# Optimization experiments

Hardware: AMD Instinct MI355X
Metric: run time of the kernel (lower is better)

## Reference

```python
import jax, jax.numpy as jnp
import numpy as np

N_HEAD = 12
N_EMBD = 768


def setup_inputs() -> dict:
    key = jax.random.key(0)
    k1, k2, k3, k4, k5 = jax.random.split(key, 5)
    B, T, C = 4, 2048, N_EMBD
    s = 0.02
    x = jax.random.normal(k1, (B, T, C), dtype=jnp.float32)
    w_attn = jax.random.normal(k2, (C, 3 * C), dtype=jnp.float32) * s
    b_attn = jnp.zeros((3 * C,), dtype=jnp.float32)
    w_proj = jax.random.normal(k3, (C, C), dtype=jnp.float32) * s
    b_proj = jnp.zeros((C,), dtype=jnp.float32)
    return {"x": x, "w_attn": w_attn, "b_attn": b_attn, "w_proj": w_proj, "b_proj": b_proj}


def reference(x, w_attn, b_attn, w_proj, b_proj):
    # dropout omitted (eval mode / dropout=0.0)
    B, T, C = x.shape
    H = N_HEAD
    D = C // H  # head dim
    qkv = x @ w_attn + b_attn                      # [B,T,3C]
    q, k, v = jnp.split(qkv, 3, axis=-1)
    q = q.reshape(B, T, H, D).transpose(0, 2, 1, 3)  # [B,H,T,D]
    k = k.reshape(B, T, H, D).transpose(0, 2, 1, 3)
    v = v.reshape(B, T, H, D).transpose(0, 2, 1, 3)
    att = jnp.einsum('bhqd,bhkd->bhqk', q, k) * (1.0 / np.sqrt(D))  # [B,H,T,T]
    causal = jnp.tril(jnp.ones((T, T), dtype=bool))
    att = jnp.where(causal[None, None], att, -jnp.inf)
    att = jax.nn.softmax(att, axis=-1)
    y = jnp.einsum('bhqk,bhkd->bhqd', att, v)      # [B,H,T,D]
    y = y.transpose(0, 2, 1, 3).reshape(B, T, C)
    return y @ w_proj + b_proj
```

## Files before the change

kernel.cpp:

```cpp
#include <hip/hip_runtime.h>
#include <stdint.h>

typedef unsigned short ushort_t;

#define T_SEQ 2048
#define BATCH 4
#define NHEAD 12
#define CEMB 768
#define HDIM 64
#define C3 2304

__device__ __forceinline__ ushort_t f2b_hw(float f) {
  union { __bf16 h; ushort_t u; } p;
  p.h = (__bf16)f;
  return p.u;
}
__device__ __forceinline__ uint32_t pkbf16(float lo, float hi) {
  union { __bf16 h[2]; uint32_t u; } p;
  p.h[0] = (__bf16)lo; p.h[1] = (__bf16)hi;
  return p.u;
}

typedef __attribute__((address_space(3))) unsigned int lds_u32_t;
typedef const __attribute__((address_space(1))) unsigned int glb_u32_t;
__device__ __forceinline__ void async_cp16(const void* g, void* l) {
  __builtin_amdgcn_global_load_lds((glb_u32_t*)g, (lds_u32_t*)l, 16, 0, 0);
}

__global__ __launch_bounds__(256) void prep_k(const float* __restrict__ x, ushort_t* __restrict__ xb,
                                              const float* __restrict__ wa, ushort_t* __restrict__ wT,
                                              const float* __restrict__ wp, ushort_t* __restrict__ wpT) {
  const int blk = blockIdx.x;
  const int tid = threadIdx.x;
  if (blk < 3072) {
    const int i = blk * 256 + tid;
    float4 a = ((const float4*)x)[2 * i];
    float4 b = ((const float4*)x)[2 * i + 1];
    uint4 v;
    v.x = pkbf16(a.x, a.y); v.y = pkbf16(a.z, a.w);
    v.z = pkbf16(b.x, b.y); v.w = pkbf16(b.z, b.w);
    ((uint4*)xb)[i] = v;
    return;
  }
  __shared__ ushort_t tile[32][33];
  const float* in; ushort_t* out; int R, C, bx, by;
  if (blk < 4800) {
    const int t = blk - 3072;
    in = wa; out = wT; R = CEMB; C = C3;
    bx = t % 72; by = t / 72;
  } else {
    const int t = blk - 4800;
    in = wp; out = wpT; R = CEMB; C = CEMB;
    bx = t % 24; by = t / 24;
  }
  const int tx = tid & 31, ty = tid >> 5;
  const int c0 = bx * 32, r0 = by * 32;
  for (int i = ty; i < 32; i += 8)
    tile[i][tx] = f2b_hw(in[(size_t)(r0 + i) * C + c0 + tx]);
  __syncthreads();
  for (int i = ty; i < 32; i += 8)
    out[(size_t)(c0 + i) * R + r0 + tx] = tile[tx][i];
}

typedef __bf16 bf16x8 __attribute__((ext_vector_type(8)));
typedef float f32x4 __attribute__((ext_vector_type(4)));

template <bool OUTF, int BM>
__global__ __launch_bounds__(256) void gemm_bt(const ushort_t* __restrict__ A,
                                               const ushort_t* __restrict__ Bt,
                                               const float* __restrict__ bias,
                                               void* __restrict__ Cv,
                                               int M, int N, int K) {
  constexpr int TM = BM / 32;
  __shared__ ushort_t As[2][BM * 32];
  __shared__ ushort_t Bs[2][128 * 32];
  const int tid = threadIdx.x;
  const int m0 = blockIdx.y * BM, n0 = blockIdx.x * 128;
  const int wid = tid >> 6, lane = tid & 63;
  const int quad = lane >> 4, l15 = lane & 15;
  const int wm = (wid >> 1) * (BM / 2), wn = (wid & 1) * 64;
  f32x4 acc[TM][4] = {};

  const int e0 = tid * 8;
  const int r0s = e0 >> 5, c0s = e0 & 31;
  const int e1 = e0 + 2048;
  const int r1s = e1 >> 5, c1s = e1 & 31;

  const int KS = K >> 5;

#define GSTAGE(ks, bf)                                                              \
  {                                                                                 \
    const int kc = (ks) << 5;                                                       \
    async_cp16(&A[(size_t)(m0 + r0s) * K + kc + c0s], &As[bf][e0]);                 \
    if constexpr (BM == 128)                                                        \
      async_cp16(&A[(size_t)(m0 + r1s) * K + kc + c1s], &As[bf][e1]);               \
    async_cp16(&Bt[(size_t)(n0 + r0s) * K + kc + c0s], &Bs[bf][e0]);                \
    async_cp16(&Bt[(size_t)(n0 + r1s) * K + kc + c1s], &Bs[bf][e1]);                \
  }

  GSTAGE(0, 0);
  for (int ks = 0; ks < KS; ks++) {
    const int pb = ks & 1;
    __syncthreads();
    if (ks + 1 < KS) GSTAGE(ks + 1, pb ^ 1);
    bf16x8 af[TM], bfr[4];
#pragma unroll
    for (int t = 0; t < TM; t++)
      af[t] = *(const bf16x8*)&As[pb][(wm + t * 16 + l15) * 32 + quad * 8];
#pragma unroll
    for (int t = 0; t < 4; t++)
      bfr[t] = *(const bf16x8*)&Bs[pb][(wn + t * 16 + l15) * 32 + quad * 8];
#pragma unroll
    for (int tm = 0; tm < TM; tm++)
#pragma unroll
      for (int tn = 0; tn < 4; tn++)
        acc[tm][tn] = __builtin_amdgcn_mfma_f32_16x16x32_bf16(af[tm], bfr[tn], acc[tm][tn], 0, 0, 0);
  }
#undef GSTAGE

#pragma unroll
  for (int tm = 0; tm < TM; tm++) {
    const int row = m0 + wm + tm * 16 + quad * 4;
#pragma unroll
    for (int tn = 0; tn < 4; tn++) {
      const int col = n0 + wn + tn * 16 + l15;
      const float bv = bias[col];
#pragma unroll
      for (int rr = 0; rr < 4; rr++) {
        if constexpr (OUTF)
          ((float*)Cv)[(size_t)(row + rr) * N + col] = acc[tm][tn][rr] + bv;
        else
          ((ushort_t*)Cv)[(size_t)(row + rr) * N + col] = f2b_hw(acc[tm][tn][rr] + bv);
      }
    }
  }
}

#define VSTR 64

__device__ __forceinline__ void commit_v(ushort_t* __restrict__ vt, const int* __restrict__ offs,
                                         uint4 pV0, uint4 pV1) {
  union { uint32_t u[4]; uint4 v; } a, c;
  a.v = pV0; c.v = pV1;
#pragma unroll
  for (int j = 0; j < 8; j++) {
    uint32_t pk = __builtin_amdgcn_perm(c.u[j >> 1], a.u[j >> 1],
                                        (j & 1) ? 0x07060302u : 0x05040100u);
    *(uint32_t*)&vt[offs[j]] = pk;
  }
}

__global__ __launch_bounds__(256, 3) void attn_mfma_k(const ushort_t* __restrict__ qkv,
                                                      ushort_t* __restrict__ y) {
  __shared__ ushort_t Ksm[2][2][64 * 32];
  __shared__ ushort_t Vt[2][64 * VSTR];

  const int qt = 15 - blockIdx.y;
  const int h = blockIdx.x >> 2, b = blockIdx.x & 3;
  const int tid = threadIdx.x;
  const int w = tid >> 6, lane = tid & 63;
  const int quad = lane >> 4, l15 = lane & 15;
  const int nkt = 2 * qt + 2;
  const int qw = qt * 128 + w * 32;

  const int e0 = tid * 8;
  const int p_slot = tid >> 2;
  const int key_true = ((p_slot >> 5) << 5) | (((p_slot >> 2) & 3) << 3) |
                       (((p_slot >> 4) & 1) << 2) | (p_slot & 3);
  const int kchunk = (tid & 3) ^ ((p_slot >> 1) & 3);
  const ushort_t* kbase = qkv + ((size_t)(b * T_SEQ) + key_true) * C3 + CEMB + h * HDIM + kchunk * 8;
  const int vpair = tid & 31, vd0 = (tid >> 5) * 8;
  const ushort_t* vbase = qkv + ((size_t)(b * T_SEQ) + 2 * vpair) * C3 + 2 * CEMB + h * HDIM + vd0;
  const size_t step = (size_t)64 * C3;

  int voffw[8];
#pragma unroll
  for (int j = 0; j < 8; j++)
    voffw[j] = (vd0 + j) * VSTR + (((vpair >> 2) ^ j) << 3) + ((vpair & 3) << 1);

  const int sw7 = l15 & 7;
  int koff[4];
#pragma unroll
  for (int m = 0; m < 4; m++)
    koff[m] = (m * 16 + l15) * 32 + ((quad ^ ((l15 >> 1) & 3)) << 3);
  int vroff[2][4];
#pragma unroll
  for (int a2 = 0; a2 < 2; a2++)
#pragma unroll
    for (int nd = 0; nd < 4; nd++)
      vroff[a2][nd] = (nd * 16 + l15) * VSTR + (((4 * a2 + quad) ^ sw7) << 3);

  const int qrel0 = w * 32 + l15;
  const int qrel1 = qrel0 + 16;

  const float C2 = 0.18033688011112042f;

  bf16x8 qB[2][2];
#pragma unroll
  for (int qf = 0; qf < 2; qf++)
#pragma unroll
    for (int kb = 0; kb < 2; kb++)
      qB[qf][kb] = *(const bf16x8*)&qkv[((size_t)(b * T_SEQ + qw + qf * 16 + l15)) * C3 +
                                        h * HDIM + kb * 32 + quad * 8];

  f32x4 o2[2][4] = {};
  float m0 = -3e38f, m1 = -3e38f;
  float lq0 = 0.f, lq1 = 0.f;

  const ushort_t* kp = kbase;
  const ushort_t* vp = vbase;
  uint4 pV0 = *(const uint4*)vp, pV1 = *(const uint4*)(vp + C3);
  async_cp16(kp, &Ksm[0][0][e0]);
  async_cp16(kp + 32, &Ksm[0][1][e0]);
  commit_v(Vt[0], voffw, pV0, pV1);
  vp += step;
  pV0 = *(const uint4*)vp; pV1 = *(const uint4*)(vp + C3);

  for (int kt = 0; kt < nkt; ++kt) {
    __syncthreads();
    if (kt + 1 < nkt) {
      const int nb = (kt + 1) & 1;
      kp += step;
      async_cp16(kp, &Ksm[nb][0][e0]);
      async_cp16(kp + 32, &Ksm[nb][1][e0]);
      commit_v(Vt[nb], voffw, pV0, pV1);
      if (kt + 2 < nkt) {
        vp += step;
        pV0 = *(const uint4*)vp; pV1 = *(const uint4*)(vp + C3);
      }
    }
    const int cb = kt & 1;

    bf16x8 kA[4][2];
#pragma unroll
    for (int m = 0; m < 4; m++) {
      kA[m][0] = *(const bf16x8*)&Ksm[cb][0][koff[m]];
      kA[m][1] = *(const bf16x8*)&Ksm[cb][1][koff[m]];
    }
    f32x4 st0[4] = {}, st1[4] = {};
#pragma unroll
    for (int m = 0; m < 4; m++) {
      st0[m] = __builtin_amdgcn_mfma_f32_16x16x32_bf16(kA[m][0], qB[0][0], st0[m], 0, 0, 0);
      st0[m] = __builtin_amdgcn_mfma_f32_16x16x32_bf16(kA[m][1], qB[0][1], st0[m], 0, 0, 0);
      st1[m] = __builtin_amdgcn_mfma_f32_16x16x32_bf16(kA[m][0], qB[1][0], st1[m], 0, 0, 0);
      st1[m] = __builtin_amdgcn_mfma_f32_16x16x32_bf16(kA[m][1], qB[1][1], st1[m], 0, 0, 0);
    }

    if (kt >= nkt - 2) {
      const int kb0 = (kt << 6) - (qt << 7) + quad * 8;
#pragma unroll
      for (int m = 0; m < 4; m++) {
        const int bm = kb0 + ((m >> 1) << 5) + ((m & 1) << 2);
#pragma unroll
        for (int r = 0; r < 4; r++) {
          const int kr = bm + r;
          if (kr > qrel0) st0[m][r] = -3e38f;
          if (kr > qrel1) st1[m][r] = -3e38f;
        }
      }
    }

    f32x4 mq0, mq1;
#pragma unroll
    for (int r = 0; r < 4; r++) {
      mq0[r] = fmaxf(fmaxf(st0[0][r], st0[1][r]), fmaxf(st0[2][r], st0[3][r]));
      mq1[r] = fmaxf(fmaxf(st1[0][r], st1[1][r]), fmaxf(st1[2][r], st1[3][r]));
    }
    const float mx0 = fmaxf(fmaxf(mq0[0], mq0[1]), fmaxf(mq0[2], mq0[3]));
    const float mx1 = fmaxf(fmaxf(mq1[0], mq1[1]), fmaxf(mq1[2], mq1[3]));

    float al0 = 1.f, al1 = 1.f;
    const bool viol = (mx0 - m0 > 22.18f) || (mx1 - m1 > 22.18f);
    if (__any(viol)) {
      float a = fmaxf(mx0, __shfl_xor(mx0, 16, 64));
      a = fmaxf(a, __shfl_xor(a, 32, 64));
      float bm = fmaxf(mx1, __shfl_xor(mx1, 16, 64));
      bm = fmaxf(bm, __shfl_xor(bm, 32, 64));
      const float n0 = fmaxf(m0, a), n1 = fmaxf(m1, bm);
      al0 = exp2f((m0 - n0) * C2);
      al1 = exp2f((m1 - n1) * C2);
      m0 = n0; m1 = n1;
#pragma unroll
      for (int nd = 0; nd < 4; nd++)
#pragma unroll
        for (int r = 0; r < 4; r++) {
          o2[0][nd][r] *= al0;
          o2[1][nd][r] *= al1;
        }
    }
    const float mnc0 = m0 * C2, mnc1 = m1 * C2;
#pragma unroll
    for (int m = 0; m < 4; m++)
#pragma unroll
      for (int r = 0; r < 4; r++) {
        st0[m][r] = exp2f(fmaf(st0[m][r], C2, -mnc0));
        st1[m][r] = exp2f(fmaf(st1[m][r], C2, -mnc1));
      }
    f32x4 s40, s41;
#pragma unroll
    for (int r = 0; r < 4; r++) {
      s40[r] = (st0[0][r] + st0[1][r]) + (st0[2][r] + st0[3][r]);
      s41[r] = (st1[0][r] + st1[1][r]) + (st1[2][r] + st1[3][r]);
    }
    lq0 = fmaf(lq0, al0, (s40[0] + s40[1]) + (s40[2] + s40[3]));
    lq1 = fmaf(lq1, al1, (s41[0] + s41[1]) + (s41[2] + s41[3]));

    bf16x8 pf0[2], pf1[2];
#pragma unroll
    for (int a2 = 0; a2 < 2; a2++) {
      union { uint32_t u[4]; bf16x8 v; } pa, pb;
      pa.u[0] = pkbf16(st0[2 * a2][0], st0[2 * a2][1]);
      pa.u[1] = pkbf16(st0[2 * a2][2], st0[2 * a2][3]);
      pa.u[2] = pkbf16(st0[2 * a2 + 1][0], st0[2 * a2 + 1][1]);
      pa.u[3] = pkbf16(st0[2 * a2 + 1][2], st0[2 * a2 + 1][3]);
      pb.u[0] = pkbf16(st1[2 * a2][0], st1[2 * a2][1]);
      pb.u[1] = pkbf16(st1[2 * a2][2], st1[2 * a2][3]);
      pb.u[2] = pkbf16(st1[2 * a2 + 1][0], st1[2 * a2 + 1][1]);
      pb.u[3] = pkbf16(st1[2 * a2 + 1][2], st1[2 * a2 + 1][3]);
      pf0[a2] = pa.v; pf1[a2] = pb.v;
    }

#pragma unroll
    for (int a2 = 0; a2 < 2; a2++)
#pragma unroll
      for (int nd = 0; nd < 4; nd++) {
        const bf16x8 vv = *(const bf16x8*)&Vt[cb][vroff[a2][nd]];
        o2[0][nd] = __builtin_amdgcn_mfma_f32_16x16x32_bf16(vv, pf0[a2], o2[0][nd], 0, 0, 0);
        o2[1][nd] = __builtin_amdgcn_mfma_f32_16x16x32_bf16(vv, pf1[a2], o2[1][nd], 0, 0, 0);
      }
  }

  {
    float lt0 = lq0 + __shfl_xor(lq0, 16, 64);
    lt0 += __shfl_xor(lt0, 32, 64);
    float lt1 = lq1 + __shfl_xor(lq1, 16, 64);
    lt1 += __shfl_xor(lt1, 32, 64);
    const float inv0 = 1.0f / lt0, inv1 = 1.0f / lt1;
#pragma unroll
    for (int qf = 0; qf < 2; qf++) {
      const float inv = qf ? inv1 : inv0;
      const int qg = qw + qf * 16 + l15;
      ushort_t* yp = y + ((size_t)(b * T_SEQ + qg)) * CEMB + h * HDIM + quad * 4;
#pragma unroll
      for (int nd = 0; nd < 4; nd++) {
        uint2 pk;
        pk.x = pkbf16(o2[qf][nd][0] * inv, o2[qf][nd][1] * inv);
        pk.y = pkbf16(o2[qf][nd][2] * inv, o2[qf][nd][3] * inv);
        *(uint2*)(yp + nd * 16) = pk;
      }
    }
  }
}

extern "C" void kernel_launch(void* const* d_in, const int* in_sizes, int n_in,
                              void* d_out, int out_size, void* d_ws, size_t ws_size,
                              hipStream_t stream) {
  const float* x      = (const float*)d_in[0];
  const float* w_attn = (const float*)d_in[1];
  const float* b_attn = (const float*)d_in[2];
  const float* w_proj = (const float*)d_in[3];
  const float* b_proj = (const float*)d_in[4];
  float* out = (float*)d_out;

  char* ws = (char*)d_ws;
  ushort_t* qkv = (ushort_t*)ws;
  ushort_t* y   = qkv + (size_t)8192 * 2304;
  ushort_t* xb  = y + (size_t)8192 * 768;
  ushort_t* wT  = xb + (size_t)8192 * 768;
  ushort_t* wpT = wT + (size_t)2304 * 768;

  prep_k<<<5376, 256, 0, stream>>>(x, xb, w_attn, wT, w_proj, wpT);

  gemm_bt<false, 128><<<dim3(C3 / 128, 8192 / 128), 256, 0, stream>>>(xb, wT, b_attn, qkv, 8192, C3, CEMB);

  attn_mfma_k<<<dim3(48, 16), 256, 0, stream>>>(qkv, y);

  gemm_bt<true, 64><<<dim3(CEMB / 128, 8192 / 64), 256, 0, stream>>>(y, wpT, b_proj, out, 8192, CEMB, CEMB);
}
```

Baseline: 221.2 us.

## Shrink attention query tile to 64 rows with 2-wave blocks

```diff
diff --git a/kernel.cpp b/kernel.cpp
--- a/kernel.cpp
+++ b/kernel.cpp
@@ -150,28 +150,29 @@
   }
 }
 
-__global__ __launch_bounds__(256, 3) void attn_mfma_k(const ushort_t* __restrict__ qkv,
+__global__ __launch_bounds__(128, 2) void attn_mfma_k(const ushort_t* __restrict__ qkv,
                                                       ushort_t* __restrict__ y) {
   __shared__ ushort_t Ksm[2][2][64 * 32];
   __shared__ ushort_t Vt[2][64 * VSTR];
 
-  const int qt = 15 - blockIdx.y;
+  const int qt = 31 - blockIdx.y;
   const int h = blockIdx.x >> 2, b = blockIdx.x & 3;
   const int tid = threadIdx.x;
   const int w = tid >> 6, lane = tid & 63;
   const int quad = lane >> 4, l15 = lane & 15;
-  const int nkt = 2 * qt + 2;
-  const int qw = qt * 128 + w * 32;
+  const int nkt = qt + 1;
+  const int qw = qt * 64 + w * 32;
 
   const int e0 = tid * 8;
   const int p_slot = tid >> 2;
   const int key_true = ((p_slot >> 5) << 5) | (((p_slot >> 2) & 3) << 3) |
                        (((p_slot >> 4) & 1) << 2) | (p_slot & 3);
-  const int kchunk = (tid & 3) ^ ((p_slot >> 1) & 3);
+  const int kchunk = (tid & 3) ^ ((tid >> 3) & 3);
   const ushort_t* kbase = qkv + ((size_t)(b * T_SEQ) + key_true) * C3 + CEMB + h * HDIM + kchunk * 8;
-  const int vpair = tid & 31, vd0 = (tid >> 5) * 8;
+  const int vpair = tid & 31, vd0 = ((tid >> 5) & 3) * 8;
   const ushort_t* vbase = qkv + ((size_t)(b * T_SEQ) + 2 * vpair) * C3 + 2 * CEMB + h * HDIM + vd0;
   const size_t step = (size_t)64 * C3;
+  const size_t krow32 = (size_t)32 * C3;
 
   int voffw[8];
 #pragma unroll
@@ -207,26 +208,44 @@
   float m0 = -3e38f, m1 = -3e38f;
   float lq0 = 0.f, lq1 = 0.f;
 
+#define KSTAGE(buf)                                          \
+  {                                                          \
+    async_cp16(kp, &Ksm[buf][0][e0]);                        \
+    async_cp16(kp + krow32, &Ksm[buf][0][e0 + 1024]);        \
+    async_cp16(kp + 32, &Ksm[buf][1][e0]);                   \
+    async_cp16(kp + krow32 + 32, &Ksm[buf][1][e0 + 1024]);   \
+  }
+#define VLOAD()                                              \
+  {                                                          \
+    pV0 = *(const uint4*)vp; pV1 = *(const uint4*)(vp + C3); \
+    pV0b = *(const uint4*)(vp + 32);                         \
+    pV1b = *(const uint4*)(vp + C3 + 32);                    \
+  }
+#define VCOMMIT(buf)                                         \
+  {                                                          \
+    commit_v(Vt[buf], voffw, pV0, pV1);                      \
+    commit_v(&Vt[buf][32 * VSTR], voffw, pV0b, pV1b);        \
+  }
+
   const ushort_t* kp = kbase;
   const ushort_t* vp = vbase;
-  uint4 pV0 = *(const uint4*)vp, pV1 = *(const uint4*)(vp + C3);
-  async_cp16(kp, &Ksm[0][0][e0]);
-  async_cp16(kp + 32, &Ksm[0][1][e0]);
-  commit_v(Vt[0], voffw, pV0, pV1);
+  uint4 pV0, pV1, pV0b, pV1b;
+  VLOAD();
+  KSTAGE(0);
+  VCOMMIT(0);
   vp += step;
-  pV0 = *(const uint4*)vp; pV1 = *(const uint4*)(vp + C3);
+  VLOAD();
 
   for (int kt = 0; kt < nkt; ++kt) {
     __syncthreads();
     if (kt + 1 < nkt) {
       const int nb = (kt + 1) & 1;
       kp += step;
-      async_cp16(kp, &Ksm[nb][0][e0]);
-      async_cp16(kp + 32, &Ksm[nb][1][e0]);
-      commit_v(Vt[nb], voffw, pV0, pV1);
+      KSTAGE(nb);
+      VCOMMIT(nb);
       if (kt + 2 < nkt) {
         vp += step;
-        pV0 = *(const uint4*)vp; pV1 = *(const uint4*)(vp + C3);
+        VLOAD();
       }
     }
     const int cb = kt & 1;
@@ -246,8 +265,8 @@
       st1[m] = __builtin_amdgcn_mfma_f32_16x16x32_bf16(kA[m][1], qB[1][1], st1[m], 0, 0, 0);
     }
 
-    if (kt >= nkt - 2) {
-      const int kb0 = (kt << 6) - (qt << 7) + quad * 8;
+    if (kt == nkt - 1) {
+      const int kb0 = quad * 8;
 #pragma unroll
       for (int m = 0; m < 4; m++) {
         const int bm = kb0 + ((m >> 1) << 5) + ((m & 1) << 2);
@@ -329,6 +348,9 @@
         o2[1][nd] = __builtin_amdgcn_mfma_f32_16x16x32_bf16(vv, pf1[a2], o2[1][nd], 0, 0, 0);
       }
   }
+#undef KSTAGE
+#undef VLOAD
+#undef VCOMMIT
 
   {
     float lt0 = lq0 + __shfl_xor(lq0, 16, 64);
@@ -373,7 +395,7 @@
 
   gemm_bt<false, 128><<<dim3(C3 / 128, 8192 / 128), 256, 0, stream>>>(xb, wT, b_attn, qkv, 8192, C3, CEMB);
 
-  attn_mfma_k<<<dim3(48, 16), 256, 0, stream>>>(qkv, y);
+  attn_mfma_k<<<dim3(48, 32), 128, 0, stream>>>(qkv, y);
 
   gemm_bt<true, 64><<<dim3(CEMB / 128, 8192 / 64), 256, 0, stream>>>(y, wpT, b_proj, out, 8192, CEMB, CEMB);
 }
```

New measurement: 239.3 us. +8.2%, slower.

## Halve attention query tile to 64 rows, doubling grid and occupancy

Applied to the files above, without the earlier changes.

```diff
diff --git a/kernel.cpp b/kernel.cpp
--- a/kernel.cpp
+++ b/kernel.cpp
@@ -150,18 +150,18 @@
   }
 }
 
-__global__ __launch_bounds__(256, 3) void attn_mfma_k(const ushort_t* __restrict__ qkv,
+__global__ __launch_bounds__(256, 5) void attn_mfma_k(const ushort_t* __restrict__ qkv,
                                                       ushort_t* __restrict__ y) {
   __shared__ ushort_t Ksm[2][2][64 * 32];
   __shared__ ushort_t Vt[2][64 * VSTR];
 
-  const int qt = 15 - blockIdx.y;
+  const int qt = 31 - blockIdx.y;
   const int h = blockIdx.x >> 2, b = blockIdx.x & 3;
   const int tid = threadIdx.x;
   const int w = tid >> 6, lane = tid & 63;
   const int quad = lane >> 4, l15 = lane & 15;
-  const int nkt = 2 * qt + 2;
-  const int qw = qt * 128 + w * 32;
+  const int nkt = qt + 1;
+  const int qw = qt * 64 + w * 16;
 
   const int e0 = tid * 8;
   const int p_slot = tid >> 2;
@@ -190,22 +190,19 @@
     for (int nd = 0; nd < 4; nd++)
       vroff[a2][nd] = (nd * 16 + l15) * VSTR + (((4 * a2 + quad) ^ sw7) << 3);
 
-  const int qrel0 = w * 32 + l15;
-  const int qrel1 = qrel0 + 16;
+  const int qrel = w * 16 + l15;
 
   const float C2 = 0.18033688011112042f;
 
-  bf16x8 qB[2][2];
-#pragma unroll
-  for (int qf = 0; qf < 2; qf++)
-#pragma unroll
-    for (int kb = 0; kb < 2; kb++)
-      qB[qf][kb] = *(const bf16x8*)&qkv[((size_t)(b * T_SEQ + qw + qf * 16 + l15)) * C3 +
-                                        h * HDIM + kb * 32 + quad * 8];
-
-  f32x4 o2[2][4] = {};
-  float m0 = -3e38f, m1 = -3e38f;
-  float lq0 = 0.f, lq1 = 0.f;
+  bf16x8 qB[2];
+#pragma unroll
+  for (int kb = 0; kb < 2; kb++)
+    qB[kb] = *(const bf16x8*)&qkv[((size_t)(b * T_SEQ + qw + l15)) * C3 +
+                                  h * HDIM + kb * 32 + quad * 8];
+
+  f32x4 o2[4] = {};
+  float m0 = -3e38f;
+  float lq0 = 0.f;
 
   const ushort_t* kp = kbase;
   const ushort_t* vp = vbase;
@@ -237,87 +234,63 @@
       kA[m][0] = *(const bf16x8*)&Ksm[cb][0][koff[m]];
       kA[m][1] = *(const bf16x8*)&Ksm[cb][1][koff[m]];
     }
-    f32x4 st0[4] = {}, st1[4] = {};
+    f32x4 st0[4] = {};
 #pragma unroll
     for (int m = 0; m < 4; m++) {
-      st0[m] = __builtin_amdgcn_mfma_f32_16x16x32_bf16(kA[m][0], qB[0][0], st0[m], 0, 0, 0);
-      st0[m] = __builtin_amdgcn_mfma_f32_16x16x32_bf16(kA[m][1], qB[0][1], st0[m], 0, 0, 0);
-      st1[m] = __builtin_amdgcn_mfma_f32_16x16x32_bf16(kA[m][0], qB[1][0], st1[m], 0, 0, 0);
-      st1[m] = __builtin_amdgcn_mfma_f32_16x16x32_bf16(kA[m][1], qB[1][1], st1[m], 0, 0, 0);
-    }
-
-    if (kt >= nkt - 2) {
-      const int kb0 = (kt << 6) - (qt << 7) + quad * 8;
+      st0[m] = __builtin_amdgcn_mfma_f32_16x16x32_bf16(kA[m][0], qB[0], st0[m], 0, 0, 0);
+      st0[m] = __builtin_amdgcn_mfma_f32_16x16x32_bf16(kA[m][1], qB[1], st0[m], 0, 0, 0);
+    }
+
+    if (kt == nkt - 1) {
+      const int kb0 = quad * 8;
 #pragma unroll
       for (int m = 0; m < 4; m++) {
         const int bm = kb0 + ((m >> 1) << 5) + ((m & 1) << 2);
 #pragma unroll
-        for (int r = 0; r < 4; r++) {
-          const int kr = bm + r;
-          if (kr > qrel0) st0[m][r] = -3e38f;
-          if (kr > qrel1) st1[m][r] = -3e38f;
-        }
+        for (int r = 0; r < 4; r++)
+          if (bm + r > qrel) st0[m][r] = -3e38f;
       }
     }
 
-    f32x4 mq0, mq1;
-#pragma unroll
-    for (int r = 0; r < 4; r++) {
+    f32x4 mq0;
+#pragma unroll
+    for (int r = 0; r < 4; r++)
       mq0[r] = fmaxf(fmaxf(st0[0][r], st0[1][r]), fmaxf(st0[2][r], st0[3][r]));
-      mq1[r] = fmaxf(fmaxf(st1[0][r], st1[1][r]), fmaxf(st1[2][r], st1[3][r]));
-    }
     const float mx0 = fmaxf(fmaxf(mq0[0], mq0[1]), fmaxf(mq0[2], mq0[3]));
-    const float mx1 = fmaxf(fmaxf(mq1[0], mq1[1]), fmaxf(mq1[2], mq1[3]));
-
-    float al0 = 1.f, al1 = 1.f;
-    const bool viol = (mx0 - m0 > 22.18f) || (mx1 - m1 > 22.18f);
-    if (__any(viol)) {
+
+    float al0 = 1.f;
+    if (__any(mx0 - m0 > 22.18f)) {
       float a = fmaxf(mx0, __shfl_xor(mx0, 16, 64));
       a = fmaxf(a, __shfl_xor(a, 32, 64));
-      float bm = fmaxf(mx1, __shfl_xor(mx1, 16, 64));
-      bm = fmaxf(bm, __shfl_xor(bm, 32, 64));
-      const float n0 = fmaxf(m0, a), n1 = fmaxf(m1, bm);
+      const float n0 = fmaxf(m0, a);
       al0 = exp2f((m0 - n0) * C2);
-      al1 = exp2f((m1 - n1) * C2);
-      m0 = n0; m1 = n1;
+      m0 = n0;
 #pragma unroll
       for (int nd = 0; nd < 4; nd++)
 #pragma unroll
-        for (int r = 0; r < 4; r++) {
-          o2[0][nd][r] *= al0;
-          o2[1][nd][r] *= al1;
-        }
-    }
-    const float mnc0 = m0 * C2, mnc1 = m1 * C2;
+        for (int r = 0; r < 4; r++) o2[nd][r] *= al0;
+    }
+    const float mnc0 = m0 * C2;
 #pragma unroll
     for (int m = 0; m < 4; m++)
 #pragma unroll
-      for (int r = 0; r < 4; r++) {
+      for (int r = 0; r < 4; r++)
         st0[m][r] = exp2f(fmaf(st0[m][r], C2, -mnc0));
-        st1[m][r] = exp2f(fmaf(st1[m][r], C2, -mnc1));
-      }
-    f32x4 s40, s41;
-#pragma unroll
-    for (int r = 0; r < 4; r++) {
+    f32x4 s40;
+#pragma unroll
+    for (int r = 0; r < 4; r++)
       s40[r] = (st0[0][r] + st0[1][r]) + (st0[2][r] + st0[3][r]);
-      s41[r] = (st1[0][r] + st1[1][r]) + (st1[2][r] + st1[3][r]);
-    }
     lq0 = fmaf(lq0, al0, (s40[0] + s40[1]) + (s40[2] + s40[3]));
-    lq1 = fmaf(lq1, al1, (s41[0] + s41[1]) + (s41[2] + s41[3]));
-
-    bf16x8 pf0[2], pf1[2];
+
+    bf16x8 pf0[2];
 #pragma unroll
     for (int a2 = 0; a2 < 2; a2++) {
-      union { uint32_t u[4]; bf16x8 v; } pa, pb;
+      union { uint32_t u[4]; bf16x8 v; } pa;
       pa.u[0] = pkbf16(st0[2 * a2][0], st0[2 * a2][1]);
       pa.u[1] = pkbf16(st0[2 * a2][2], st0[2 * a2][3]);
       pa.u[2] = pkbf16(st0[2 * a2 + 1][0], st0[2 * a2 + 1][1]);
       pa.u[3] = pkbf16(st0[2 * a2 + 1][2], st0[2 * a2 + 1][3]);
-      pb.u[0] = pkbf16(st1[2 * a2][0], st1[2 * a2][1]);
-      pb.u[1] = pkbf16(st1[2 * a2][2], st1[2 * a2][3]);
-      pb.u[2] = pkbf16(st1[2 * a2 + 1][0], st1[2 * a2 + 1][1]);
-      pb.u[3] = pkbf16(st1[2 * a2 + 1][2], st1[2 * a2 + 1][3]);
-      pf0[a2] = pa.v; pf1[a2] = pb.v;
+      pf0[a2] = pa.v;
     }
 
 #pragma unroll
@@ -325,29 +298,22 @@
 #pragma unroll
       for (int nd = 0; nd < 4; nd++) {
         const bf16x8 vv = *(const bf16x8*)&Vt[cb][vroff[a2][nd]];
-        o2[0][nd] = __builtin_amdgcn_mfma_f32_16x16x32_bf16(vv, pf0[a2], o2[0][nd], 0, 0, 0);
-        o2[1][nd] = __builtin_amdgcn_mfma_f32_16x16x32_bf16(vv, pf1[a2], o2[1][nd], 0, 0, 0);
+        o2[nd] = __builtin_amdgcn_mfma_f32_16x16x32_bf16(vv, pf0[a2], o2[nd], 0, 0, 0);
       }
   }
 
   {
     float lt0 = lq0 + __shfl_xor(lq0, 16, 64);
     lt0 += __shfl_xor(lt0, 32, 64);
-    float lt1 = lq1 + __shfl_xor(lq1, 16, 64);
-    lt1 += __shfl_xor(lt1, 32, 64);
-    const float inv0 = 1.0f / lt0, inv1 = 1.0f / lt1;
-#pragma unroll
-    for (int qf = 0; qf < 2; qf++) {
-      const float inv = qf ? inv1 : inv0;
-      const int qg = qw + qf * 16 + l15;
-      ushort_t* yp = y + ((size_t)(b * T_SEQ + qg)) * CEMB + h * HDIM + quad * 4;
-#pragma unroll
-      for (int nd = 0; nd < 4; nd++) {
-        uint2 pk;
-        pk.x = pkbf16(o2[qf][nd][0] * inv, o2[qf][nd][1] * inv);
-        pk.y = pkbf16(o2[qf][nd][2] * inv, o2[qf][nd][3] * inv);
-        *(uint2*)(yp + nd * 16) = pk;
-      }
+    const float inv = 1.0f / lt0;
+    const int qg = qw + l15;
+    ushort_t* yp = y + ((size_t)(b * T_SEQ + qg)) * CEMB + h * HDIM + quad * 4;
+#pragma unroll
+    for (int nd = 0; nd < 4; nd++) {
+      uint2 pk;
+      pk.x = pkbf16(o2[nd][0] * inv, o2[nd][1] * inv);
+      pk.y = pkbf16(o2[nd][2] * inv, o2[nd][3] * inv);
+      *(uint2*)(yp + nd * 16) = pk;
     }
   }
 }
@@ -373,7 +339,7 @@
 
   gemm_bt<false, 128><<<dim3(C3 / 128, 8192 / 128), 256, 0, stream>>>(xb, wT, b_attn, qkv, 8192, C3, CEMB);
 
-  attn_mfma_k<<<dim3(48, 16), 256, 0, stream>>>(qkv, y);
+  attn_mfma_k<<<dim3(48, 32), 256, 0, stream>>>(qkv, y);
 
   gemm_bt<true, 64><<<dim3(CEMB / 128, 8192 / 64), 256, 0, stream>>>(y, wpT, b_proj, out, 8192, CEMB, CEMB);
 }
```

Result: faster. 215.4 us (-2.6%).
